# Performance work log

Hardware: AMD Instinct MI355X
Metric: run time of the kernel (lower is better)

The kernel has to match this reference:

```python
import jax, jax.numpy as jnp
import numpy as np

B, S, E, H = 8, 2048, 256, 8
LN_EPS = 1e-5


def setup_inputs() -> dict:
    key = jax.random.key(0)
    ks = jax.random.split(key, 5)
    x = jax.random.normal(ks[0], (B, S, E), dtype=jnp.float32)
    Wq = jax.random.normal(ks[1], (E, E), dtype=jnp.float32) * 0.02
    Wk = jax.random.normal(ks[2], (E, E), dtype=jnp.float32) * 0.02
    Wv = jax.random.normal(ks[3], (E, E), dtype=jnp.float32) * 0.02
    bias_table = jax.random.normal(ks[4], (2 * S - 1, H), dtype=jnp.float32) * 0.02
    ln_gamma = jnp.ones((E,), dtype=jnp.float32)
    ln_beta = jnp.zeros((E,), dtype=jnp.float32)
    return {"x": x, "Wq": Wq, "Wk": Wk, "Wv": Wv,
            "bias_table": bias_table, "ln_gamma": ln_gamma, "ln_beta": ln_beta}


def reference(x, Wq, Wk, Wv, bias_table, ln_gamma, ln_beta):
    b, s, e = x.shape
    h = bias_table.shape[1]
    d = e // h
    scale = e ** (-0.5)  # note: original scales by emb_size**-0.5, not head_dim

    # torch nn.Linear(bias=False): y = x @ W.T
    q = (x @ Wq.T).reshape(b, s, h, d).transpose(0, 2, 1, 3)  # [b,h,s,d]
    k = (x @ Wk.T).reshape(b, s, h, d).transpose(0, 2, 1, 3)
    v = (x @ Wv.T).reshape(b, s, h, d).transpose(0, 2, 1, 3)

    # full attention matrix (the chunked torch loop computes exactly this)
    attn = jax.nn.softmax(jnp.einsum('bhqd,bhkd->bhqk', q, k) * scale, axis=-1)

    # relative bias: index[i,j] = i - j + (s-1); added AFTER softmax (faithful)
    idx = jnp.arange(s)[:, None] - jnp.arange(s)[None, :] + (s - 1)  # [s,s]
    rel_bias = bias_table[idx].transpose(2, 0, 1)  # [h,s,s]
    attn = attn + rel_bias[None]

    out = jnp.einsum('bhqk,bhkd->bhqd', attn, v)
    out = out.transpose(0, 2, 1, 3).reshape(b, s, e)

    # LayerNorm over last dim
    mu = jnp.mean(out, axis=-1, keepdims=True)
    var = jnp.var(out, axis=-1, keepdims=True)
    out = (out - mu) * jax.lax.rsqrt(var + LN_EPS) * ln_gamma + ln_beta
    return out
```

## Files before the change

### kernel.cpp

```cpp
#include <hip/hip_runtime.h>
#include <math.h>

typedef unsigned short u16;
typedef unsigned int u32;
typedef __attribute__((ext_vector_type(2))) __fp16 half2;
typedef __attribute__((ext_vector_type(8))) __fp16 half8;
typedef __attribute__((ext_vector_type(16))) float floatx16;

constexpr int CB = 8;
constexpr int CS = 2048;
constexpr int CE = 256;
constexpr int CH = 8;
constexpr int CD = 32;
constexpr float CLN_EPS = 1e-5f;
constexpr float QSC = 0.0625f * 1.44269504088896341f;

constexpr int QP = 40;
constexpr int VP = 72;
constexpr int XP = 268;
constexpr int RST = 4104;

__device__ inline u32 fbits(float f) { union { float f; u32 u; } c; c.f = f; return c.u; }
__device__ inline u32 pkrtz(float a, float b) {
  half2 h = __builtin_amdgcn_cvt_pkrtz(a, b);
  union { half2 h; u32 u; } c; c.h = h; return c.u;
}
__device__ inline u16 h1(float a) {
  union { __fp16 h; u16 u; } c; c.h = (__fp16)a; return c.u;
}
__device__ inline half8 ldh8(const u16* p) {
  union { uint4 q; half8 v; } c; c.q = *(const uint4*)p; return c.v;
}

#if __has_builtin(__builtin_amdgcn_permlane32_swap)
__device__ inline void swap32(u32& a, u32& b) {
  typedef __attribute__((ext_vector_type(2))) unsigned int uint2v;
  uint2v r = __builtin_amdgcn_permlane32_swap(a, b, false, false);
  a = r[0]; b = r[1];
}
#else
__device__ inline void swap32(u32& a, u32& b) {
  int hi = (threadIdx.x >> 5) & 1;
  u32 sa = (u32)__shfl_xor((int)a, 32);
  u32 sb = (u32)__shfl_xor((int)b, 32);
  u32 na = hi ? sb : a;
  u32 nb = hi ? b : sa;
  a = na; b = nb;
}
#endif

__global__ __launch_bounds__(256) void prep_kernel(
    const float* __restrict__ Wq, const float* __restrict__ Wk,
    const float* __restrict__ Wv, const float* __restrict__ table,
    u16* __restrict__ Wb, u16* __restrict__ revg) {
  int gid = blockIdx.x * 256 + threadIdx.x;
  if (gid < 49152) {
    int which = gid >> 14;
    int off = (gid & 16383) * 4;
    const float* W = (which == 0) ? Wq : (which == 1) ? Wk : Wv;
    float4 f = *(const float4*)&W[off];
    uint2 o; o.x = pkrtz(f.x, f.y); o.y = pkrtz(f.z, f.w);
    *(uint2*)&Wb[(size_t)which * CE * CE + off] = o;
  } else {
    int gid2 = gid - 49152;
    if (gid2 >= 64 * 513) return;
    int g = gid2 / 513;
    int j0 = (gid2 - g * 513) * 8;
    int h = g >> 3, p = g & 7;
    u16 vals[8];
#pragma unroll
    for (int t = 0; t < 8; ++t) {
      int src = 4094 - (j0 + t + p);
      vals[t] = (src >= 0) ? h1(table[(size_t)src * CH + h]) : (u16)0;
    }
    *(uint4*)&revg[(size_t)g * RST + j0] = *(uint4*)vals;
  }
}

__global__ __launch_bounds__(256, 4) void qkv_mfma_kernel(
    const float* __restrict__ x, const u16* __restrict__ Wb,
    u16* __restrict__ qb, u16* __restrict__ kb, u16* __restrict__ vb) {
  __shared__ __attribute__((aligned(16))) u16 Xs[64 * XP];
  const int m0 = blockIdx.x * 64;
  const int which = blockIdx.y;
  const int tid = threadIdx.x;
  const int lane = tid & 63, wv = tid >> 6;
  const int lm = lane & 31, lg = lane >> 5;

#pragma unroll
  for (int it = 0; it < 16; ++it) {
    int c = tid + 256 * it;
    int row = c >> 6, f4 = c & 63;
    float4 f = *(const float4*)&x[(size_t)(m0 + row) * CE + f4 * 4];
    uint2 o; o.x = pkrtz(f.x, f.y); o.y = pkrtz(f.z, f.w);
    *(uint2*)&Xs[row * XP + f4 * 4] = o;
  }
  __syncthreads();

  const u16* Wsrc = Wb + (size_t)which * CE * CE;

#pragma unroll
  for (int r = 0; r < 2; ++r) {
    const int F = wv * 32 + r * 128;
    floatx16 acc0, acc1;
#pragma unroll
    for (int i = 0; i < 16; ++i) { acc0[i] = 0.f; acc1[i] = 0.f; }
#pragma unroll
    for (int kt = 0; kt < 16; ++kt) {
      half8 wfr = ldh8(&Wsrc[(size_t)(F + lm) * CE + kt * 16 + lg * 8]);
      half8 b0 = ldh8(&Xs[lm * XP + kt * 16 + lg * 8]);
      half8 b1 = ldh8(&Xs[(32 + lm) * XP + kt * 16 + lg * 8]);
      acc0 = __builtin_amdgcn_mfma_f32_32x32x16_f16(wfr, b0, acc0, 0, 0, 0);
      acc1 = __builtin_amdgcn_mfma_f32_32x32x16_f16(wfr, b1, acc1, 0, 0, 0);
    }
    const int hh = F >> 5;
#pragma unroll
    for (int ms = 0; ms < 2; ++ms) {
      floatx16& acc = ms ? acc1 : acc0;
      const int sg = m0 + ms * 32 + lm;
      const int bI = sg >> 11, sI = sg & (CS - 1);
      if (which < 2) {
        u16* dst = which ? kb : qb;
        float scl = which ? 1.0f : QSC;
        u32 D[8];
#pragma unroll
        for (int g = 0; g < 8; ++g)
          D[g] = pkrtz(acc[2 * g] * scl, acc[2 * g + 1] * scl);
        swap32(D[0], D[2]); swap32(D[1], D[3]);
        swap32(D[4], D[6]); swap32(D[5], D[7]);
        size_t base = (((size_t)bI * CH + hh) * CS + sI) * CD;
        uint4 U0; U0.x = D[0]; U0.y = D[1]; U0.z = D[2]; U0.w = D[3];
        uint4 U1; U1.x = D[4]; U1.y = D[5]; U1.z = D[6]; U1.w = D[7];
        *(uint4*)&dst[base + 8 * lg] = U0;
        *(uint4*)&dst[base + 16 + 8 * lg] = U1;
      } else {
#pragma unroll
        for (int rg = 0; rg < 16; ++rg) {
          int d = (rg & 3) + 8 * (rg >> 2) + 4 * lg;
          vb[(((size_t)bI * CH + hh) * CD + d) * CS + sI] = h1(acc[rg]);
        }
      }
    }
  }
}

__global__ __launch_bounds__(256, 4) void attn_mfma_kernel(
    const u16* __restrict__ qm, const u16* __restrict__ km,
    const u16* __restrict__ vm, const u16* __restrict__ revg,
    float* __restrict__ out) {
  __shared__ __attribute__((aligned(16))) u16 Ks[2][64 * QP];
  __shared__ __attribute__((aligned(16))) u16 Vt[2][32 * VP];

  const int q0 = blockIdx.x * 128;
  const int bh = blockIdx.y;
  const int b = bh >> 3, h = bh & 7;
  const int tid = threadIdx.x;
  const int lane = tid & 63, wv = tid >> 6;
  const int lm = lane & 31, lg = lane >> 5;
  const u16* qbp = qm + (size_t)bh * CS * CD;
  const u16* kbp = km + (size_t)bh * CS * CD;
  const u16* vbp = vm + (size_t)bh * CD * CS;

  const int qrow = wv * 32 + lm;
  const u16* qp = qbp + (size_t)(q0 + qrow) * CD;
  half8 qa0 = ldh8(qp + lg * 8);
  half8 qa1 = ldh8(qp + 16 + lg * 8);

  const int Xb = 2047 - q0 - qrow + lg * 8;
  const int pp = Xb & 7;
  const u16* bp = revg + (size_t)(h * 8 + pp) * RST + (Xb - pp);

  const int krow = tid >> 2, kch = tid & 3;
  const int vrow = tid >> 3, vch = tid & 7;
  uint4 kreg = *(const uint4*)&kbp[(size_t)krow * CD + kch * 8];
  uint4 vreg = *(const uint4*)&vbp[(size_t)vrow * CS + vch * 8];

  const half2 PC3 = {(__fp16)0.0558022f, (__fp16)0.0558022f};
  const half2 PC2 = {(__fp16)0.2401997f, (__fp16)0.2401997f};
  const half2 PC1 = {(__fp16)0.6931472f, (__fp16)0.6931472f};
  const half2 PC0 = {(__fp16)1.0f, (__fp16)1.0f};

  floatx16 acc_e, acc_b;
#pragma unroll
  for (int i = 0; i < 16; ++i) { acc_e[i] = 0.f; acc_b[i] = 0.f; }
  float l = 0.f;

  for (int k0 = 0; k0 < CS; k0 += 64) {
    const int p = (k0 >> 6) & 1;
    *(uint4*)&Ks[p][krow * QP + kch * 8] = kreg;
    *(uint4*)&Vt[p][vrow * VP + vch * 8] = vreg;
    if (k0 + 64 < CS) {
      kreg = *(const uint4*)&kbp[(size_t)(k0 + 64 + krow) * CD + kch * 8];
      vreg = *(const uint4*)&vbp[(size_t)vrow * CS + (k0 + 64) + vch * 8];
    }
    uint4 bu0 = *(const uint4*)&bp[k0];
    uint4 bu1 = *(const uint4*)&bp[k0 + 16];
    uint4 bu2 = *(const uint4*)&bp[k0 + 32];
    uint4 bu3 = *(const uint4*)&bp[k0 + 48];
    __syncthreads();

    floatx16 sc0, sc1;
#pragma unroll
    for (int i = 0; i < 16; ++i) { sc0[i] = 0.f; sc1[i] = 0.f; }
    {
      half8 a00 = ldh8(&Ks[p][lm * QP + lg * 8]);
      half8 a01 = ldh8(&Ks[p][lm * QP + 16 + lg * 8]);
      half8 a10 = ldh8(&Ks[p][(32 + lm) * QP + lg * 8]);
      half8 a11 = ldh8(&Ks[p][(32 + lm) * QP + 16 + lg * 8]);
      sc0 = __builtin_amdgcn_mfma_f32_32x32x16_f16(a00, qa0, sc0, 0, 0, 0);
      sc0 = __builtin_amdgcn_mfma_f32_32x32x16_f16(a01, qa1, sc0, 0, 0, 0);
      sc1 = __builtin_amdgcn_mfma_f32_32x32x16_f16(a10, qa0, sc1, 0, 0, 0);
      sc1 = __builtin_amdgcn_mfma_f32_32x32x16_f16(a11, qa1, sc1, 0, 0, 0);
    }

    half2 lacc = {(__fp16)0.0f, (__fp16)0.0f};
#pragma unroll
    for (int ct = 0; ct < 2; ++ct) {
      floatx16& sc = ct ? sc1 : sc0;
      u32 P[8];
#pragma unroll
      for (int g = 0; g < 8; ++g) {
        half2 xv = __builtin_amdgcn_cvt_pkrtz(sc[2 * g], sc[2 * g + 1]);
        half2 r = __builtin_elementwise_fma(PC3, xv, PC2);
        r = __builtin_elementwise_fma(r, xv, PC1);
        r = __builtin_elementwise_fma(r, xv, PC0);
        lacc += r;
        union { half2 h; u32 u; } cc; cc.h = r;
        P[g] = cc.u;
      }
      swap32(P[0], P[2]); swap32(P[1], P[3]);
      swap32(P[4], P[6]); swap32(P[5], P[7]);
      union { u32 u[4]; half8 v; } B0, B1;
      B0.u[0] = P[0]; B0.u[1] = P[1]; B0.u[2] = P[2]; B0.u[3] = P[3];
      B1.u[0] = P[4]; B1.u[1] = P[5]; B1.u[2] = P[6]; B1.u[3] = P[7];
      half8 va0 = ldh8(&Vt[p][lm * VP + ct * 32 + lg * 8]);
      half8 va1 = ldh8(&Vt[p][lm * VP + ct * 32 + 16 + lg * 8]);
      acc_e = __builtin_amdgcn_mfma_f32_32x32x16_f16(va0, B0.v, acc_e, 0, 0, 0);
      acc_e = __builtin_amdgcn_mfma_f32_32x32x16_f16(va1, B1.v, acc_e, 0, 0, 0);
      union { uint4 q; half8 v; } Bb0, Bb1;
      Bb0.q = ct ? bu2 : bu0;
      Bb1.q = ct ? bu3 : bu1;
      acc_b = __builtin_amdgcn_mfma_f32_32x32x16_f16(va0, Bb0.v, acc_b, 0, 0, 0);
      acc_b = __builtin_amdgcn_mfma_f32_32x32x16_f16(va1, Bb1.v, acc_b, 0, 0, 0);
    }
    l += (float)lacc[0] + (float)lacc[1];
  }

  l += __shfl_xor(l, 32);
  float rl = __builtin_amdgcn_rcpf(l);
  size_t ob = ((size_t)b * CS + q0 + qrow) * CE + h * CD;
#pragma unroll
  for (int g = 0; g < 4; ++g) {
    float4 r4;
    r4.x = acc_e[4 * g + 0] * rl + acc_b[4 * g + 0];
    r4.y = acc_e[4 * g + 1] * rl + acc_b[4 * g + 1];
    r4.z = acc_e[4 * g + 2] * rl + acc_b[4 * g + 2];
    r4.w = acc_e[4 * g + 3] * rl + acc_b[4 * g + 3];
    *(float4*)&out[ob + 8 * g + 4 * lg] = r4;
  }
}

__global__ __launch_bounds__(256) void ln_kernel(float* __restrict__ io,
                                                 const float* __restrict__ gamma,
                                                 const float* __restrict__ beta) {
  int tid = threadIdx.x;
  size_t row = (size_t)blockIdx.x * 4 + (tid >> 6);
  int c = (tid & 63) * 4;
  float4 v = *(const float4*)&io[row * CE + c];
  float s1 = v.x + v.y + v.z + v.w;
  float s2 = v.x * v.x + v.y * v.y + v.z * v.z + v.w * v.w;
#pragma unroll
  for (int off = 1; off < 64; off <<= 1) {
    s1 += __shfl_xor(s1, off);
    s2 += __shfl_xor(s2, off);
  }
  float mu = s1 * (1.0f / CE);
  float var = s2 * (1.0f / CE) - mu * mu;
  float rs = rsqrtf(var + CLN_EPS);
  float4 g = *(const float4*)&gamma[c];
  float4 be = *(const float4*)&beta[c];
  float4 o;
  o.x = (v.x - mu) * rs * g.x + be.x;
  o.y = (v.y - mu) * rs * g.y + be.y;
  o.z = (v.z - mu) * rs * g.z + be.z;
  o.w = (v.w - mu) * rs * g.w + be.w;
  *(float4*)&io[row * CE + c] = o;
}

extern "C" void kernel_launch(void* const* d_in, const int* in_sizes, int n_in,
                              void* d_out, int out_size, void* d_ws, size_t ws_size,
                              hipStream_t stream) {
  (void)in_sizes; (void)n_in; (void)out_size; (void)ws_size;
  const float* x          = (const float*)d_in[0];
  const float* Wq         = (const float*)d_in[1];
  const float* Wk         = (const float*)d_in[2];
  const float* Wv         = (const float*)d_in[3];
  const float* bias_table = (const float*)d_in[4];
  const float* gamma      = (const float*)d_in[5];
  const float* beta       = (const float*)d_in[6];
  float* out = (float*)d_out;

  u16* ws = (u16*)d_ws;
  u16* Wb = ws;
  u16* qb = Wb + 3 * CE * CE;
  u16* kb = qb + (size_t)CB * CH * CS * CD;
  u16* vb = kb + (size_t)CB * CH * CS * CD;
  u16* revg = vb + (size_t)CB * CH * CS * CD;

  prep_kernel<<<dim3(321), dim3(256), 0, stream>>>(Wq, Wk, Wv, bias_table, Wb, revg);
  qkv_mfma_kernel<<<dim3(256, 3), dim3(256), 0, stream>>>(x, Wb, qb, kb, vb);
  attn_mfma_kernel<<<dim3(CS / 128, CB * CH), dim3(256), 0, stream>>>(qb, kb, vb, revg, out);
  ln_kernel<<<dim3(CB * CS / 4), dim3(256), 0, stream>>>(out, gamma, beta);
}
```

Baseline: 173.6 us.

## Drop LDS staging in attention; each wave handles two query subtiles from direct loads

The attention kernel no longer stages K and V tiles through double-buffered shared memory with __syncthreads. Each wave now loads K and V fragments straight from global memory (relying on cache) and reuses them across two 32-row query subtiles, so each block covers 256 queries. The grid becomes 1D with bh in the low bits so neighbouring blocks share the same head's K/V in L2. s_setprio is placed around the MFMA groups, and launch bounds drop to 2 blocks per CU to allow the doubled accumulators. The aim is to remove barrier and LDS traffic, at the cost of more redundant global/L2 loads, higher register pressure and lower occupancy.

```diff
diff --git a/kernel.cpp b/kernel.cpp
--- a/kernel.cpp
+++ b/kernel.cpp
@@ -15,8 +15,6 @@
 constexpr float CLN_EPS = 1e-5f;
 constexpr float QSC = 0.0625f * 1.44269504088896341f;
 
-constexpr int QP = 40;
-constexpr int VP = 72;
 constexpr int XP = 268;
 constexpr int RST = 4104;
 
@@ -144,15 +142,13 @@
   }
 }
 
-__global__ __launch_bounds__(256, 4) void attn_mfma_kernel(
+__global__ __launch_bounds__(256, 2) void attn_mfma_kernel(
     const u16* __restrict__ qm, const u16* __restrict__ km,
     const u16* __restrict__ vm, const u16* __restrict__ revg,
     float* __restrict__ out) {
-  __shared__ __attribute__((aligned(16))) u16 Ks[2][64 * QP];
-  __shared__ __attribute__((aligned(16))) u16 Vt[2][32 * VP];
-
-  const int q0 = blockIdx.x * 128;
-  const int bh = blockIdx.y;
+  const int id = blockIdx.x;
+  const int bh = id & 63;
+  const int q0 = (id >> 6) * 256;
   const int b = bh >> 3, h = bh & 7;
   const int tid = threadIdx.x;
   const int lane = tid & 63, wv = tid >> 6;
@@ -161,102 +157,118 @@
   const u16* kbp = km + (size_t)bh * CS * CD;
   const u16* vbp = vm + (size_t)bh * CD * CS;
 
-  const int qrow = wv * 32 + lm;
-  const u16* qp = qbp + (size_t)(q0 + qrow) * CD;
-  half8 qa0 = ldh8(qp + lg * 8);
-  half8 qa1 = ldh8(qp + 16 + lg * 8);
-
-  const int Xb = 2047 - q0 - qrow + lg * 8;
-  const int pp = Xb & 7;
-  const u16* bp = revg + (size_t)(h * 8 + pp) * RST + (Xb - pp);
-
-  const int krow = tid >> 2, kch = tid & 3;
-  const int vrow = tid >> 3, vch = tid & 7;
-  uint4 kreg = *(const uint4*)&kbp[(size_t)krow * CD + kch * 8];
-  uint4 vreg = *(const uint4*)&vbp[(size_t)vrow * CS + vch * 8];
+  const int qrA = wv * 64 + lm, qrB = qrA + 32;
+  const u16* qpA = qbp + (size_t)(q0 + qrA) * CD;
+  const u16* qpB = qbp + (size_t)(q0 + qrB) * CD;
+  half8 qa0A = ldh8(qpA + lg * 8), qa1A = ldh8(qpA + 16 + lg * 8);
+  half8 qa0B = ldh8(qpB + lg * 8), qa1B = ldh8(qpB + 16 + lg * 8);
+
+  const int XbA = 2047 - q0 - qrA + lg * 8;
+  const int ppA = XbA & 7;
+  const u16* bpA = revg + (size_t)(h * 8 + ppA) * RST + (XbA - ppA);
+  const int XbB = XbA - 32;
+  const int ppB = XbB & 7;
+  const u16* bpB = revg + (size_t)(h * 8 + ppB) * RST + (XbB - ppB);
 
   const half2 PC3 = {(__fp16)0.0558022f, (__fp16)0.0558022f};
   const half2 PC2 = {(__fp16)0.2401997f, (__fp16)0.2401997f};
   const half2 PC1 = {(__fp16)0.6931472f, (__fp16)0.6931472f};
   const half2 PC0 = {(__fp16)1.0f, (__fp16)1.0f};
 
-  floatx16 acc_e, acc_b;
-#pragma unroll
-  for (int i = 0; i < 16; ++i) { acc_e[i] = 0.f; acc_b[i] = 0.f; }
-  float l = 0.f;
+  floatx16 zf;
+#pragma unroll
+  for (int i = 0; i < 16; ++i) zf[i] = 0.f;
+  floatx16 aeA = zf, abA = zf, aeB = zf, abB = zf;
+  float lA = 0.f, lB = 0.f;
+
+#define SUBTILE(QA0, QA1, BU0, BU1, BU2, BU3, AE, AB, LL)                        \
+  {                                                                              \
+    __builtin_amdgcn_s_setprio(1);                                               \
+    floatx16 sc0 = __builtin_amdgcn_mfma_f32_32x32x16_f16(a00, QA0, zf, 0, 0, 0);\
+    sc0 = __builtin_amdgcn_mfma_f32_32x32x16_f16(a01, QA1, sc0, 0, 0, 0);        \
+    floatx16 sc1 = __builtin_amdgcn_mfma_f32_32x32x16_f16(a10, QA0, zf, 0, 0, 0);\
+    sc1 = __builtin_amdgcn_mfma_f32_32x32x16_f16(a11, QA1, sc1, 0, 0, 0);        \
+    __builtin_amdgcn_s_setprio(0);                                               \
+    half2 lacc = {(__fp16)0.0f, (__fp16)0.0f};                                   \
+    _Pragma("unroll")                                                            \
+    for (int ct = 0; ct < 2; ++ct) {                                             \
+      floatx16& sc = ct ? sc1 : sc0;                                             \
+      u32 P[8];                                                                  \
+      _Pragma("unroll")                                                          \
+      for (int g = 0; g < 8; ++g) {                                              \
+        half2 xv = __builtin_amdgcn_cvt_pkrtz(sc[2 * g], sc[2 * g + 1]);         \
+        half2 r = __builtin_elementwise_fma(PC3, xv, PC2);                       \
+        r = __builtin_elementwise_fma(r, xv, PC1);                               \
+        r = __builtin_elementwise_fma(r, xv, PC0);                               \
+        lacc += r;                                                               \
+        union { half2 hh; u32 u; } cc; cc.hh = r;                                \
+        P[g] = cc.u;                                                             \
+      }                                                                          \
+      swap32(P[0], P[2]); swap32(P[1], P[3]);                                    \
+      swap32(P[4], P[6]); swap32(P[5], P[7]);                                    \
+      union { u32 u[4]; half8 v; } B0, B1;                                       \
+      B0.u[0] = P[0]; B0.u[1] = P[1]; B0.u[2] = P[2]; B0.u[3] = P[3];            \
+      B1.u[0] = P[4]; B1.u[1] = P[5]; B1.u[2] = P[6]; B1.u[3] = P[7];            \
+      half8 va0 = ct ? va10 : va00;                                              \
+      half8 va1 = ct ? va11 : va01;                                              \
+      union { uint4 q; half8 v; } Bb0, Bb1;                                      \
+      Bb0.q = ct ? BU2 : BU0;                                                    \
+      Bb1.q = ct ? BU3 : BU1;                                                    \
+      __builtin_amdgcn_s_setprio(1);                                             \
+      AE = __builtin_amdgcn_mfma_f32_32x32x16_f16(va0, B0.v, AE, 0, 0, 0);       \
+      AE = __builtin_amdgcn_mfma_f32_32x32x16_f16(va1, B1.v, AE, 0, 0, 0);       \
+      AB = __builtin_amdgcn_mfma_f32_32x32x16_f16(va0, Bb0.v, AB, 0, 0, 0);      \
+      AB = __builtin_amdgcn_mfma_f32_32x32x16_f16(va1, Bb1.v, AB, 0, 0, 0);      \
+      __builtin_amdgcn_s_setprio(0);                                             \
+    }                                                                            \
+    LL += (float)lacc[0] + (float)lacc[1];                                       \
+  }
 
   for (int k0 = 0; k0 < CS; k0 += 64) {
-    const int p = (k0 >> 6) & 1;
-    *(uint4*)&Ks[p][krow * QP + kch * 8] = kreg;
-    *(uint4*)&Vt[p][vrow * VP + vch * 8] = vreg;
-    if (k0 + 64 < CS) {
-      kreg = *(const uint4*)&kbp[(size_t)(k0 + 64 + krow) * CD + kch * 8];
-      vreg = *(const uint4*)&vbp[(size_t)vrow * CS + (k0 + 64) + vch * 8];
-    }
-    uint4 bu0 = *(const uint4*)&bp[k0];
-    uint4 bu1 = *(const uint4*)&bp[k0 + 16];
-    uint4 bu2 = *(const uint4*)&bp[k0 + 32];
-    uint4 bu3 = *(const uint4*)&bp[k0 + 48];
-    __syncthreads();
-
-    floatx16 sc0, sc1;
-#pragma unroll
-    for (int i = 0; i < 16; ++i) { sc0[i] = 0.f; sc1[i] = 0.f; }
-    {
-      half8 a00 = ldh8(&Ks[p][lm * QP + lg * 8]);
-      half8 a01 = ldh8(&Ks[p][lm * QP + 16 + lg * 8]);
-      half8 a10 = ldh8(&Ks[p][(32 + lm) * QP + lg * 8]);
-      half8 a11 = ldh8(&Ks[p][(32 + lm) * QP + 16 + lg * 8]);
-      sc0 = __builtin_amdgcn_mfma_f32_32x32x16_f16(a00, qa0, sc0, 0, 0, 0);
-      sc0 = __builtin_amdgcn_mfma_f32_32x32x16_f16(a01, qa1, sc0, 0, 0, 0);
-      sc1 = __builtin_amdgcn_mfma_f32_32x32x16_f16(a10, qa0, sc1, 0, 0, 0);
-      sc1 = __builtin_amdgcn_mfma_f32_32x32x16_f16(a11, qa1, sc1, 0, 0, 0);
-    }
-
-    half2 lacc = {(__fp16)0.0f, (__fp16)0.0f};
-#pragma unroll
-    for (int ct = 0; ct < 2; ++ct) {
-      floatx16& sc = ct ? sc1 : sc0;
-      u32 P[8];
-#pragma unroll
-      for (int g = 0; g < 8; ++g) {
-        half2 xv = __builtin_amdgcn_cvt_pkrtz(sc[2 * g], sc[2 * g + 1]);
-        half2 r = __builtin_elementwise_fma(PC3, xv, PC2);
-        r = __builtin_elementwise_fma(r, xv, PC1);
-        r = __builtin_elementwise_fma(r, xv, PC0);
-        lacc += r;
-        union { half2 h; u32 u; } cc; cc.h = r;
-        P[g] = cc.u;
-      }
-      swap32(P[0], P[2]); swap32(P[1], P[3]);
-      swap32(P[4], P[6]); swap32(P[5], P[7]);
-      union { u32 u[4]; half8 v; } B0, B1;
-      B0.u[0] = P[0]; B0.u[1] = P[1]; B0.u[2] = P[2]; B0.u[3] = P[3];
-      B1.u[0] = P[4]; B1.u[1] = P[5]; B1.u[2] = P[6]; B1.u[3] = P[7];
-      half8 va0 = ldh8(&Vt[p][lm * VP + ct * 32 + lg * 8]);
-      half8 va1 = ldh8(&Vt[p][lm * VP + ct * 32 + 16 + lg * 8]);
-      acc_e = __builtin_amdgcn_mfma_f32_32x32x16_f16(va0, B0.v, acc_e, 0, 0, 0);
-      acc_e = __builtin_amdgcn_mfma_f32_32x32x16_f16(va1, B1.v, acc_e, 0, 0, 0);
-      union { uint4 q; half8 v; } Bb0, Bb1;
-      Bb0.q = ct ? bu2 : bu0;
-      Bb1.q = ct ? bu3 : bu1;
-      acc_b = __builtin_amdgcn_mfma_f32_32x32x16_f16(va0, Bb0.v, acc_b, 0, 0, 0);
-      acc_b = __builtin_amdgcn_mfma_f32_32x32x16_f16(va1, Bb1.v, acc_b, 0, 0, 0);
-    }
-    l += (float)lacc[0] + (float)lacc[1];
-  }
-
-  l += __shfl_xor(l, 32);
-  float rl = __builtin_amdgcn_rcpf(l);
-  size_t ob = ((size_t)b * CS + q0 + qrow) * CE + h * CD;
+    const u16* kk = kbp + (size_t)k0 * CD;
+    half8 a00 = ldh8(kk + lm * CD + lg * 8);
+    half8 a01 = ldh8(kk + lm * CD + 16 + lg * 8);
+    half8 a10 = ldh8(kk + (32 + lm) * CD + lg * 8);
+    half8 a11 = ldh8(kk + (32 + lm) * CD + 16 + lg * 8);
+    const u16* vk = vbp + (size_t)lm * CS + k0;
+    half8 va00 = ldh8(vk + lg * 8);
+    half8 va01 = ldh8(vk + 16 + lg * 8);
+    half8 va10 = ldh8(vk + 32 + lg * 8);
+    half8 va11 = ldh8(vk + 48 + lg * 8);
+    uint4 buA0 = *(const uint4*)&bpA[k0];
+    uint4 buA1 = *(const uint4*)&bpA[k0 + 16];
+    uint4 buA2 = *(const uint4*)&bpA[k0 + 32];
+    uint4 buA3 = *(const uint4*)&bpA[k0 + 48];
+    uint4 buB0 = *(const uint4*)&bpB[k0];
+    uint4 buB1 = *(const uint4*)&bpB[k0 + 16];
+    uint4 buB2 = *(const uint4*)&bpB[k0 + 32];
+    uint4 buB3 = *(const uint4*)&bpB[k0 + 48];
+
+    SUBTILE(qa0A, qa1A, buA0, buA1, buA2, buA3, aeA, abA, lA)
+    SUBTILE(qa0B, qa1B, buB0, buB1, buB2, buB3, aeB, abB, lB)
+  }
+#undef SUBTILE
+
+  lA += __shfl_xor(lA, 32);
+  lB += __shfl_xor(lB, 32);
+  float rlA = __builtin_amdgcn_rcpf(lA);
+  float rlB = __builtin_amdgcn_rcpf(lB);
+  size_t obA = ((size_t)b * CS + q0 + qrA) * CE + h * CD;
+  size_t obB = ((size_t)b * CS + q0 + qrB) * CE + h * CD;
 #pragma unroll
   for (int g = 0; g < 4; ++g) {
     float4 r4;
-    r4.x = acc_e[4 * g + 0] * rl + acc_b[4 * g + 0];
-    r4.y = acc_e[4 * g + 1] * rl + acc_b[4 * g + 1];
-    r4.z = acc_e[4 * g + 2] * rl + acc_b[4 * g + 2];
-    r4.w = acc_e[4 * g + 3] * rl + acc_b[4 * g + 3];
-    *(float4*)&out[ob + 8 * g + 4 * lg] = r4;
+    r4.x = aeA[4 * g + 0] * rlA + abA[4 * g + 0];
+    r4.y = aeA[4 * g + 1] * rlA + abA[4 * g + 1];
+    r4.z = aeA[4 * g + 2] * rlA + abA[4 * g + 2];
+    r4.w = aeA[4 * g + 3] * rlA + abA[4 * g + 3];
+    *(float4*)&out[obA + 8 * g + 4 * lg] = r4;
+    float4 s4;
+    s4.x = aeB[4 * g + 0] * rlB + abB[4 * g + 0];
+    s4.y = aeB[4 * g + 1] * rlB + abB[4 * g + 1];
+    s4.z = aeB[4 * g + 2] * rlB + abB[4 * g + 2];
+    s4.w = aeB[4 * g + 3] * rlB + abB[4 * g + 3];
+    *(float4*)&out[obB + 8 * g + 4 * lg] = s4;
   }
 }
 
@@ -309,6 +321,6 @@
 
   prep_kernel<<<dim3(321), dim3(256), 0, stream>>>(Wq, Wk, Wv, bias_table, Wb, revg);
   qkv_mfma_kernel<<<dim3(256, 3), dim3(256), 0, stream>>>(x, Wb, qb, kb, vb);
-  attn_mfma_kernel<<<dim3(CS / 128, CB * CH), dim3(256), 0, stream>>>(qb, kb, vb, revg, out);
+  attn_mfma_kernel<<<dim3(512), dim3(256), 0, stream>>>(qb, kb, vb, revg, out);
   ln_kernel<<<dim3(CB * CS / 4), dim3(256), 0, stream>>>(out, gamma, beta);
 }
```

New measurement: 175.5 us. About the same (+1.1%).

## Process 128-key chunks per barrier, add MFMA priority hints, remap grid ordering

Applied to the files above, without the earlier changes.

The attention loop now stages two 64-key K/V tiles per iteration in double-buffered shared memory. This halves the number of __syncthreads and global prefetch rounds, and the inner loop is unrolled over the two sub-tiles. The MFMA sections are wrapped in s_setprio to favour matrix issue across waves. The grid is flattened so consecutive blocks cover different (batch, head) pairs for the same query tile, which changes L2 locality. The trade-off is doubled LDS and prefetch registers, which may reduce occupancy below the launch-bounds target.

```diff
diff --git a/kernel.cpp b/kernel.cpp
--- a/kernel.cpp
+++ b/kernel.cpp
@@ -148,11 +148,12 @@
     const u16* __restrict__ qm, const u16* __restrict__ km,
     const u16* __restrict__ vm, const u16* __restrict__ revg,
     float* __restrict__ out) {
-  __shared__ __attribute__((aligned(16))) u16 Ks[2][64 * QP];
-  __shared__ __attribute__((aligned(16))) u16 Vt[2][32 * VP];
-
-  const int q0 = blockIdx.x * 128;
-  const int bh = blockIdx.y;
+  __shared__ __attribute__((aligned(16))) u16 Ks[2][2][64 * QP];
+  __shared__ __attribute__((aligned(16))) u16 Vt[2][2][32 * VP];
+
+  const int id = blockIdx.x;
+  const int bh = id & 63;
+  const int q0 = (id >> 6) * 128;
   const int b = bh >> 3, h = bh & 7;
   const int tid = threadIdx.x;
   const int lane = tid & 63, wv = tid >> 6;
@@ -172,78 +173,89 @@
 
   const int krow = tid >> 2, kch = tid & 3;
   const int vrow = tid >> 3, vch = tid & 7;
-  uint4 kreg = *(const uint4*)&kbp[(size_t)krow * CD + kch * 8];
-  uint4 vreg = *(const uint4*)&vbp[(size_t)vrow * CS + vch * 8];
+  uint4 kr0 = *(const uint4*)&kbp[(size_t)krow * CD + kch * 8];
+  uint4 kr1 = *(const uint4*)&kbp[(size_t)(64 + krow) * CD + kch * 8];
+  uint4 vr0 = *(const uint4*)&vbp[(size_t)vrow * CS + vch * 8];
+  uint4 vr1 = *(const uint4*)&vbp[(size_t)vrow * CS + 64 + vch * 8];
 
   const half2 PC3 = {(__fp16)0.0558022f, (__fp16)0.0558022f};
   const half2 PC2 = {(__fp16)0.2401997f, (__fp16)0.2401997f};
   const half2 PC1 = {(__fp16)0.6931472f, (__fp16)0.6931472f};
   const half2 PC0 = {(__fp16)1.0f, (__fp16)1.0f};
 
-  floatx16 acc_e, acc_b;
-#pragma unroll
-  for (int i = 0; i < 16; ++i) { acc_e[i] = 0.f; acc_b[i] = 0.f; }
+  floatx16 zf;
+#pragma unroll
+  for (int i = 0; i < 16; ++i) zf[i] = 0.f;
+  floatx16 acc_e = zf, acc_b = zf;
   float l = 0.f;
 
-  for (int k0 = 0; k0 < CS; k0 += 64) {
-    const int p = (k0 >> 6) & 1;
-    *(uint4*)&Ks[p][krow * QP + kch * 8] = kreg;
-    *(uint4*)&Vt[p][vrow * VP + vch * 8] = vreg;
-    if (k0 + 64 < CS) {
-      kreg = *(const uint4*)&kbp[(size_t)(k0 + 64 + krow) * CD + kch * 8];
-      vreg = *(const uint4*)&vbp[(size_t)vrow * CS + (k0 + 64) + vch * 8];
-    }
-    uint4 bu0 = *(const uint4*)&bp[k0];
-    uint4 bu1 = *(const uint4*)&bp[k0 + 16];
-    uint4 bu2 = *(const uint4*)&bp[k0 + 32];
-    uint4 bu3 = *(const uint4*)&bp[k0 + 48];
+  for (int s0 = 0; s0 < CS; s0 += 128) {
+    const int p = (s0 >> 7) & 1;
+    *(uint4*)&Ks[p][0][krow * QP + kch * 8] = kr0;
+    *(uint4*)&Ks[p][1][krow * QP + kch * 8] = kr1;
+    *(uint4*)&Vt[p][0][vrow * VP + vch * 8] = vr0;
+    *(uint4*)&Vt[p][1][vrow * VP + vch * 8] = vr1;
+    if (s0 + 128 < CS) {
+      kr0 = *(const uint4*)&kbp[(size_t)(s0 + 128 + krow) * CD + kch * 8];
+      kr1 = *(const uint4*)&kbp[(size_t)(s0 + 192 + krow) * CD + kch * 8];
+      vr0 = *(const uint4*)&vbp[(size_t)vrow * CS + (s0 + 128) + vch * 8];
+      vr1 = *(const uint4*)&vbp[(size_t)vrow * CS + (s0 + 192) + vch * 8];
+    }
     __syncthreads();
 
-    floatx16 sc0, sc1;
-#pragma unroll
-    for (int i = 0; i < 16; ++i) { sc0[i] = 0.f; sc1[i] = 0.f; }
-    {
-      half8 a00 = ldh8(&Ks[p][lm * QP + lg * 8]);
-      half8 a01 = ldh8(&Ks[p][lm * QP + 16 + lg * 8]);
-      half8 a10 = ldh8(&Ks[p][(32 + lm) * QP + lg * 8]);
-      half8 a11 = ldh8(&Ks[p][(32 + lm) * QP + 16 + lg * 8]);
-      sc0 = __builtin_amdgcn_mfma_f32_32x32x16_f16(a00, qa0, sc0, 0, 0, 0);
+#pragma unroll
+    for (int t = 0; t < 2; ++t) {
+      const int k0 = s0 + t * 64;
+      uint4 bu0 = *(const uint4*)&bp[k0];
+      uint4 bu1 = *(const uint4*)&bp[k0 + 16];
+      uint4 bu2 = *(const uint4*)&bp[k0 + 32];
+      uint4 bu3 = *(const uint4*)&bp[k0 + 48];
+
+      half8 a00 = ldh8(&Ks[p][t][lm * QP + lg * 8]);
+      half8 a01 = ldh8(&Ks[p][t][lm * QP + 16 + lg * 8]);
+      half8 a10 = ldh8(&Ks[p][t][(32 + lm) * QP + lg * 8]);
+      half8 a11 = ldh8(&Ks[p][t][(32 + lm) * QP + 16 + lg * 8]);
+      __builtin_amdgcn_s_setprio(1);
+      floatx16 sc0 = __builtin_amdgcn_mfma_f32_32x32x16_f16(a00, qa0, zf, 0, 0, 0);
       sc0 = __builtin_amdgcn_mfma_f32_32x32x16_f16(a01, qa1, sc0, 0, 0, 0);
-      sc1 = __builtin_amdgcn_mfma_f32_32x32x16_f16(a10, qa0, sc1, 0, 0, 0);
+      floatx16 sc1 = __builtin_amdgcn_mfma_f32_32x32x16_f16(a10, qa0, zf, 0, 0, 0);
       sc1 = __builtin_amdgcn_mfma_f32_32x32x16_f16(a11, qa1, sc1, 0, 0, 0);
-    }
-
-    half2 lacc = {(__fp16)0.0f, (__fp16)0.0f};
-#pragma unroll
-    for (int ct = 0; ct < 2; ++ct) {
-      floatx16& sc = ct ? sc1 : sc0;
-      u32 P[8];
-#pragma unroll
-      for (int g = 0; g < 8; ++g) {
-        half2 xv = __builtin_amdgcn_cvt_pkrtz(sc[2 * g], sc[2 * g + 1]);
-        half2 r = __builtin_elementwise_fma(PC3, xv, PC2);
-        r = __builtin_elementwise_fma(r, xv, PC1);
-        r = __builtin_elementwise_fma(r, xv, PC0);
-        lacc += r;
-        union { half2 h; u32 u; } cc; cc.h = r;
-        P[g] = cc.u;
+      __builtin_amdgcn_s_setprio(0);
+
+      half2 lacc = {(__fp16)0.0f, (__fp16)0.0f};
+#pragma unroll
+      for (int ct = 0; ct < 2; ++ct) {
+        floatx16& sc = ct ? sc1 : sc0;
+        u32 P[8];
+#pragma unroll
+        for (int g = 0; g < 8; ++g) {
+          half2 xv = __builtin_amdgcn_cvt_pkrtz(sc[2 * g], sc[2 * g + 1]);
+          half2 r = __builtin_elementwise_fma(PC3, xv, PC2);
+          r = __builtin_elementwise_fma(r, xv, PC1);
+          r = __builtin_elementwise_fma(r, xv, PC0);
+          lacc += r;
+          union { half2 hh; u32 u; } cc; cc.hh = r;
+          P[g] = cc.u;
+        }
+        swap32(P[0], P[2]); swap32(P[1], P[3]);
+        swap32(P[4], P[6]); swap32(P[5], P[7]);
+        union { u32 u[4]; half8 v; } B0, B1;
+        B0.u[0] = P[0]; B0.u[1] = P[1]; B0.u[2] = P[2]; B0.u[3] = P[3];
+        B1.u[0] = P[4]; B1.u[1] = P[5]; B1.u[2] = P[6]; B1.u[3] = P[7];
+        half8 va0 = ldh8(&Vt[p][t][lm * VP + ct * 32 + lg * 8]);
+        half8 va1 = ldh8(&Vt[p][t][lm * VP + ct * 32 + 16 + lg * 8]);
+        union { uint4 q; half8 v; } Bb0, Bb1;
+        Bb0.q = ct ? bu2 : bu0;
+        Bb1.q = ct ? bu3 : bu1;
+        __builtin_amdgcn_s_setprio(1);
+        acc_e = __builtin_amdgcn_mfma_f32_32x32x16_f16(va0, B0.v, acc_e, 0, 0, 0);
+        acc_e = __builtin_amdgcn_mfma_f32_32x32x16_f16(va1, B1.v, acc_e, 0, 0, 0);
+        acc_b = __builtin_amdgcn_mfma_f32_32x32x16_f16(va0, Bb0.v, acc_b, 0, 0, 0);
+        acc_b = __builtin_amdgcn_mfma_f32_32x32x16_f16(va1, Bb1.v, acc_b, 0, 0, 0);
+        __builtin_amdgcn_s_setprio(0);
       }
-      swap32(P[0], P[2]); swap32(P[1], P[3]);
-      swap32(P[4], P[6]); swap32(P[5], P[7]);
-      union { u32 u[4]; half8 v; } B0, B1;
-      B0.u[0] = P[0]; B0.u[1] = P[1]; B0.u[2] = P[2]; B0.u[3] = P[3];
-      B1.u[0] = P[4]; B1.u[1] = P[5]; B1.u[2] = P[6]; B1.u[3] = P[7];
-      half8 va0 = ldh8(&Vt[p][lm * VP + ct * 32 + lg * 8]);
-      half8 va1 = ldh8(&Vt[p][lm * VP + ct * 32 + 16 + lg * 8]);
-      acc_e = __builtin_amdgcn_mfma_f32_32x32x16_f16(va0, B0.v, acc_e, 0, 0, 0);
-      acc_e = __builtin_amdgcn_mfma_f32_32x32x16_f16(va1, B1.v, acc_e, 0, 0, 0);
-      union { uint4 q; half8 v; } Bb0, Bb1;
-      Bb0.q = ct ? bu2 : bu0;
-      Bb1.q = ct ? bu3 : bu1;
-      acc_b = __builtin_amdgcn_mfma_f32_32x32x16_f16(va0, Bb0.v, acc_b, 0, 0, 0);
-      acc_b = __builtin_amdgcn_mfma_f32_32x32x16_f16(va1, Bb1.v, acc_b, 0, 0, 0);
-    }
-    l += (float)lacc[0] + (float)lacc[1];
+      l += (float)lacc[0] + (float)lacc[1];
+    }
   }
 
   l += __shfl_xor(l, 32);
@@ -309,6 +321,6 @@
 
   prep_kernel<<<dim3(321), dim3(256), 0, stream>>>(Wq, Wk, Wv, bias_table, Wb, revg);
   qkv_mfma_kernel<<<dim3(256, 3), dim3(256), 0, stream>>>(x, Wb, qb, kb, vb);
-  attn_mfma_kernel<<<dim3(CS / 128, CB * CH), dim3(256), 0, stream>>>(qb, kb, vb, revg, out);
+  attn_mfma_kernel<<<dim3(1024), dim3(256), 0, stream>>>(qb, kb, vb, revg, out);
   ln_kernel<<<dim3(CB * CS / 4), dim3(256), 0, stream>>>(out, gamma, beta);
 }
```

New measurement: 176.1 us. No clear change (+1.4%).
